# Kernel tuning notes

Measured on AMD Instinct MI355X. Metric: run time of the kernel, lower is better.

## Reference

```python
import jax, jax.numpy as jnp
import numpy as np
from jax import lax

# --- geometry constants (match init_kwargs geo) ---
NVOX = (128, 128, 128)          # (nz, ny, nx) voxels
SVOX = (256.0, 256.0, 256.0)    # volume size in mm
NDET = (256, 256)               # (V, U) detector pixels
SDET = (512.0, 512.0)           # detector size in mm
DSO = 1000.0                    # source-to-isocenter distance
DSD = 1536.0                    # source-to-detector distance
N_ANGLES = 360


def setup_inputs() -> dict:
    key = jax.random.key(0)
    # projections: [B, 1, n_angles, nDetV, nDetU]
    x = jax.random.normal(key, (2, 1, N_ANGLES, NDET[0], NDET[1]), dtype=jnp.float32)
    return {"x": x}


def _backproject(proj):
    """Voxel-driven cone-beam back-projection (adjoint of cone-beam forward projector).

    proj: [B, A, V, U] projections over a circular source trajectory.
    returns volume [B, nz, ny, nx].
    """
    B, A, V, U = proj.shape
    nz, ny, nx = NVOX
    dz, dy, dx = SVOX[0] / nz, SVOX[1] / ny, SVOX[2] / nx
    dv, du = SDET[0] / V, SDET[1] / U

    # voxel center coordinates (isocenter at origin)
    zc = ((jnp.arange(nz, dtype=jnp.float32) - (nz - 1) / 2) * dz)[:, None, None]  # [nz,1,1]
    yc = ((jnp.arange(ny, dtype=jnp.float32) - (ny - 1) / 2) * dy)[None, :, None]  # [1,ny,1]
    xc = ((jnp.arange(nx, dtype=jnp.float32) - (nx - 1) / 2) * dx)[None, None, :]  # [1,1,nx]

    angles = jnp.linspace(0.0, 2.0 * np.pi, A, endpoint=False, dtype=jnp.float32)
    proj_a = jnp.moveaxis(proj, 1, 0)  # [A, B, V, U] for scan over angles

    def bilinear(p, iv, iu):
        # p: [B, V, U]; iv, iu: [nz, ny, nx] fractional detector coords
        valid = (iu >= 0) & (iu <= U - 1) & (iv >= 0) & (iv <= V - 1)
        iu = jnp.clip(iu, 0.0, U - 1.0)
        iv = jnp.clip(iv, 0.0, V - 1.0)
        u0 = jnp.floor(iu).astype(jnp.int32)
        v0 = jnp.floor(iv).astype(jnp.int32)
        u1 = jnp.minimum(u0 + 1, U - 1)
        v1 = jnp.minimum(v0 + 1, V - 1)
        fu = iu - u0
        fv = iv - v0
        s = (p[:, v0, u0] * ((1 - fv) * (1 - fu))
             + p[:, v0, u1] * ((1 - fv) * fu)
             + p[:, v1, u0] * (fv * (1 - fu))
             + p[:, v1, u1] * (fv * fu))            # [B,nz,ny,nx]
        return s * valid.astype(p.dtype)

    def body(vol, inp):
        theta, p = inp                                # scalar, [B,V,U]
        c, s = jnp.cos(theta), jnp.sin(theta)
        xr = xc * c + yc * s                          # rotated in-plane coords [1,ny,nx]
        yr = -xc * s + yc * c                         # [1,ny,nx]
        mag = DSD / (DSO - xr)                        # perspective magnification [1,ny,nx]
        iu = jnp.broadcast_to(yr * mag / du + (U - 1) / 2, (nz, ny, nx))
        iv = zc * mag / dv + (V - 1) / 2              # [nz,ny,nx]
        vol = vol + bilinear(p, iv, iu)
        return vol, None

    vol0 = jnp.zeros((B, nz, ny, nx), dtype=proj.dtype)
    vol, _ = lax.scan(body, vol0, (angles, proj_a))
    return vol


def reference(x):
    # x: [B, 1, A, V, U] -> volume [B, 1, nz, ny, nx]
    vol = _backproject(x[:, 0])
    return vol[:, None]
```

## Files before the change

### kernel.cpp

```cpp
#include <hip/hip_runtime.h>
#include <math.h>

#define NA    360
#define ZPT   8
#define PITCH 65
#define NSTG  2048
#define VLO_MAX 224
#define ULO_MAX 191


typedef float v2f __attribute__((ext_vector_type(2)));
typedef __attribute__((address_space(1))) const void gas_t;
typedef __attribute__((address_space(3))) void las_t;

__device__ __forceinline__ int2 bbox_angle(float c, float s,
    float xclo, float xchi, float yclo, float ychi, float zvlo, float zvhi)
{
    const float a0 = xclo*c, a1 = xchi*c, b0 = yclo*s, b1 = ychi*s;
    const float xr0 = a0+b0, xr1 = a0+b1, xr2 = a1+b0, xr3 = a1+b1;
    const float xmn = fminf(fminf(xr0,xr1), fminf(xr2,xr3));
    const float xmx = fmaxf(fmaxf(xr0,xr1), fmaxf(xr2,xr3));
    const float c0 = yclo*c, c1 = ychi*c, d0 = xclo*s, d1 = xchi*s;
    const float yr0 = c0-d0, yr1 = c0-d1, yr2 = c1-d0, yr3 = c1-d1;
    const float ymn = fminf(fminf(yr0,yr1), fminf(yr2,yr3));
    const float ymx = fmaxf(fmaxf(yr0,yr1), fmaxf(yr2,yr3));
    const float mlo = 1536.f * __builtin_amdgcn_rcpf(1000.f - xmn);
    const float mhi = 1536.f * __builtin_amdgcn_rcpf(1000.f - xmx);
    const float umn = fminf(fminf(ymn*mlo, ymn*mhi), fminf(ymx*mlo, ymx*mhi));
    int u_lo = (int)floorf(fmaf(umn, 0.5f, 127.5f)) - 1;
    u_lo = u_lo < 0 ? 0 : (u_lo > ULO_MAX ? ULO_MAX : u_lo);
    const float vmn = fminf(fminf(zvlo*mlo, zvlo*mhi), fminf(zvhi*mlo, zvhi*mhi));
    int v_lo = (int)floorf(vmn + 127.5f) - 1;
    v_lo = v_lo < 0 ? 0 : (v_lo > VLO_MAX ? VLO_MAX : v_lo);
    return make_int2(u_lo, v_lo);
}

__device__ __forceinline__ void stage8(const char* gb, float* ldsw,
                                       const int goffB[8]) {
    #pragma unroll
    for (int i = 0; i < 8; ++i) {
        __builtin_amdgcn_global_load_lds(
            (gas_t*)(gb + goffB[i]),
            (las_t*)(ldsw + i * 64), 4, 0, 0);
    }
}

__device__ __forceinline__ void compute_angle(const float* __restrict__ smb,
    float c, float s, float xc, float yc, float zf0, int u_lo, int v_lo,
    v2f acc[ZPT])
{
    const float xr  = xc*c + yc*s;
    const float yr  = yc*c - xc*s;
    const float mag = 1536.f * __builtin_amdgcn_rcpf(1000.f - xr);
    const float iu  = fmaf(yr*mag, 0.5f, 127.5f);
    const bool uval = (iu >= 0.f) && (iu <= 255.f);
    const float iuc = fminf(fmaxf(iu, 0.f), 255.f);
    int u0 = (int)iuc; u0 = u0 > 254 ? 254 : u0;
    const float fu  = iuc - (float)u0;
    const float w   = uval ? 1.f : 0.f;
    const float wu1 = fu*w, wu0 = w - wu1;
    const v2f   wuv = {wu0, wu1};
    const int   ui  = u0 - u_lo;
    const float ivb = fmaf(zf0, mag, 127.5f) - (float)v_lo;
    #pragma unroll
    for (int k = 0; k < ZPT; ++k) {
        const float ivl = fmaf((float)k, mag, ivb);
        const int   v0  = (int)ivl;
        const float fv  = __builtin_amdgcn_fractf(ivl);
        const float* r  = smb + (v0 * PITCH + ui);
        v2f p0 = {r[0],     r[1]};
        v2f p1 = {r[PITCH], r[PITCH+1]};
        const v2f fvv = {fv, fv};
        const v2f q = __builtin_elementwise_fma(fvv, p1 - p0, p0);
        acc[k] = __builtin_elementwise_fma(wuv, q, acc[k]);
    }
}

__global__ __launch_bounds__(256, 4) void bp_kernel(const float* __restrict__ proj,
                                                    float* __restrict__ out) {
    __shared__ float2 cs_sh[NA];
    __shared__ int2   bb_sh[NA];
    __shared__ float  patch[2][NSTG];

    const int tid = threadIdx.y * 16 + threadIdx.x;

    const int zg = blockIdx.x;
    const int t  = blockIdx.y;
    const int b  = blockIdx.z;
    const int x0 = (t & 7) * 16;
    const int y0 = (t >> 3) * 16;
    const int zb = zg * ZPT;

    const float zf0  = (float)zb - 63.5f;
    const float xclo = ((float)x0 - 63.5f) * 2.f, xchi = xclo + 30.f;
    const float yclo = ((float)y0 - 63.5f) * 2.f, ychi = yclo + 30.f;

    for (int i = tid; i < NA; i += 256) {
        float th = (float)i * (float)(2.0 * M_PI / (double)NA);
        float sv, cv; sincosf(th, &sv, &cv);
        cs_sh[i] = make_float2(cv, sv);
        bb_sh[i] = bbox_angle(cv, sv, xclo, xchi, yclo, ychi, zf0, zf0 + 7.f);
    }
    __syncthreads();

    const int wv   = tid >> 6;
    const int lane = tid & 63;
    int goffB[8];
    #pragma unroll
    for (int i = 0; i < 8; ++i) {
        const int flat = wv * 512 + i * 64 + lane;
        const int r  = flat / PITCH;
        const int cc = flat - r * PITCH;
        goffB[i] = (r * 256 + cc) * 4;
    }

    const char* projB = (const char*)(proj + (size_t)b * (NA * 65536));
    const float xc = ((float)(x0 + threadIdx.x) - 63.5f) * 2.f;
    const float yc = ((float)(y0 + threadIdx.y) - 63.5f) * 2.f;

    float* l0 = &patch[0][wv * 512];
    float* l1 = &patch[1][wv * 512];

    v2f acc[ZPT];
    #pragma unroll
    for (int k = 0; k < ZPT; ++k) acc[k] = (v2f){0.f, 0.f};

    {
        const int2 lo = bb_sh[0];
        const uint32_t aoff = __builtin_amdgcn_readfirstlane(
            ((uint32_t)lo.y << 10) + ((uint32_t)lo.x << 2));
        stage8(projB + aoff, l0, goffB);
    }
    __syncthreads();

    for (int a = 0; a < NA; a += 2) {
        {
            const int2 lo = bb_sh[a + 1];
            const uint32_t aoff = __builtin_amdgcn_readfirstlane(
                (uint32_t)(a + 1) * 262144u +
                ((uint32_t)lo.y << 10) + ((uint32_t)lo.x << 2));
            stage8(projB + aoff, l1, goffB);
        }
        {
            const float2 cs = cs_sh[a];
            const int2   lo = bb_sh[a];
            compute_angle(patch[0], cs.x, cs.y, xc, yc, zf0, lo.x, lo.y, acc);
        }
        __syncthreads();
        if (a + 2 < NA) {
            const int2 lo = bb_sh[a + 2];
            const uint32_t aoff = __builtin_amdgcn_readfirstlane(
                (uint32_t)(a + 2) * 262144u +
                ((uint32_t)lo.y << 10) + ((uint32_t)lo.x << 2));
            stage8(projB + aoff, l0, goffB);
        }
        {
            const float2 cs = cs_sh[a + 1];
            const int2   lo = bb_sh[a + 1];
            compute_angle(patch[1], cs.x, cs.y, xc, yc, zf0, lo.x, lo.y, acc);
        }
        __syncthreads();
    }

    float* o = out + (((size_t)b * 128 + zb) * 128 + (y0 + threadIdx.y)) * 128
                   + (x0 + threadIdx.x);
    #pragma unroll
    for (int k = 0; k < ZPT; ++k) {
        o[(size_t)k * (128 * 128)] = acc[k].x + acc[k].y;
    }
}

extern "C" void kernel_launch(void* const* d_in, const int* in_sizes, int n_in,
                              void* d_out, int out_size, void* d_ws, size_t ws_size,
                              hipStream_t stream) {
    const float* proj = (const float*)d_in[0];
    float* out = (float*)d_out;
    dim3 grid(128 / ZPT, 64, 2);
    dim3 block(16, 16, 1);
    hipLaunchKernelGGL(bp_kernel, grid, block, 0, stream, proj, out);
}
```

Baseline: 843.0 us.

## Process both batches per block with interleaved LDS patch and 16-byte staging loads

Each block now handles both batch items. It stages each angle's patch from both projections into one interleaved LDS layout (rows of 128 floats, 64 columns per batch) using 16-byte global_load_lds transfers instead of 4-byte ones. The geometry, bilinear index and weight computations are shared across the two batches, and the grid is halved. The doubled LDS patch and accumulators raise register and LDS use, which may cut occupancy. The patch width drops from 65 to 64 columns, with ULO_MAX adjusted to match.

Result: faster. 785.8 us (-6.8%).

```diff
diff --git a/kernel.cpp b/kernel.cpp
--- a/kernel.cpp
+++ b/kernel.cpp
@@ -3,10 +3,10 @@
 
 #define NA    360
 #define ZPT   8
-#define PITCH 65
-#define NSTG  2048
+#define NSTG  4096
 #define VLO_MAX 224
-#define ULO_MAX 191
+#define ULO_MAX 192
+#define BSTRIDE 94371840
 
 
 typedef float v2f __attribute__((ext_vector_type(2)));
@@ -35,19 +35,19 @@
     return make_int2(u_lo, v_lo);
 }
 
-__device__ __forceinline__ void stage8(const char* gb, float* ldsw,
-                                       const int goffB[8]) {
+__device__ __forceinline__ void stage4(const char* gb, float* ldsw,
+                                       const int goffB[4]) {
     #pragma unroll
-    for (int i = 0; i < 8; ++i) {
+    for (int i = 0; i < 4; ++i) {
         __builtin_amdgcn_global_load_lds(
             (gas_t*)(gb + goffB[i]),
-            (las_t*)(ldsw + i * 64), 4, 0, 0);
+            (las_t*)(ldsw + i * 256), 16, 0, 0);
     }
 }
 
 __device__ __forceinline__ void compute_angle(const float* __restrict__ smb,
     float c, float s, float xc, float yc, float zf0, int u_lo, int v_lo,
-    v2f acc[ZPT])
+    v2f accA[ZPT], v2f accB[ZPT])
 {
     const float xr  = xc*c + yc*s;
     const float yr  = yc*c - xc*s;
@@ -67,12 +67,16 @@
         const float ivl = fmaf((float)k, mag, ivb);
         const int   v0  = (int)ivl;
         const float fv  = __builtin_amdgcn_fractf(ivl);
-        const float* r  = smb + (v0 * PITCH + ui);
-        v2f p0 = {r[0],     r[1]};
-        v2f p1 = {r[PITCH], r[PITCH+1]};
+        const float* r  = smb + ((v0 << 7) + ui);
+        const v2f a0 = {r[0],   r[1]};
+        const v2f b0 = {r[64],  r[65]};
+        const v2f a1 = {r[128], r[129]};
+        const v2f b1 = {r[192], r[193]};
         const v2f fvv = {fv, fv};
-        const v2f q = __builtin_elementwise_fma(fvv, p1 - p0, p0);
-        acc[k] = __builtin_elementwise_fma(wuv, q, acc[k]);
+        const v2f qa = __builtin_elementwise_fma(fvv, a1 - a0, a0);
+        const v2f qb = __builtin_elementwise_fma(fvv, b1 - b0, b0);
+        accA[k] = __builtin_elementwise_fma(wuv, qa, accA[k]);
+        accB[k] = __builtin_elementwise_fma(wuv, qb, accB[k]);
     }
 }
 
@@ -86,7 +90,6 @@
 
     const int zg = blockIdx.x;
     const int t  = blockIdx.y;
-    const int b  = blockIdx.z;
     const int x0 = (t & 7) * 16;
     const int y0 = (t >> 3) * 16;
     const int zb = zg * ZPT;
@@ -105,31 +108,35 @@
 
     const int wv   = tid >> 6;
     const int lane = tid & 63;
-    int goffB[8];
+    int goffB[4];
     #pragma unroll
-    for (int i = 0; i < 8; ++i) {
-        const int flat = wv * 512 + i * 64 + lane;
-        const int r  = flat / PITCH;
-        const int cc = flat - r * PITCH;
-        goffB[i] = (r * 256 + cc) * 4;
+    for (int i = 0; i < 4; ++i) {
+        const int f    = wv * 1024 + i * 256 + lane * 4;
+        const int v    = f >> 7;
+        const int bsel = (f >> 6) & 1;
+        const int col  = f & 63;
+        goffB[i] = bsel * BSTRIDE + v * 1024 + col * 4;
     }
 
-    const char* projB = (const char*)(proj + (size_t)b * (NA * 65536));
+    const char* projB = (const char*)proj;
     const float xc = ((float)(x0 + threadIdx.x) - 63.5f) * 2.f;
     const float yc = ((float)(y0 + threadIdx.y) - 63.5f) * 2.f;
 
-    float* l0 = &patch[0][wv * 512];
-    float* l1 = &patch[1][wv * 512];
+    float* l0 = &patch[0][wv * 1024];
+    float* l1 = &patch[1][wv * 1024];
 
-    v2f acc[ZPT];
+    v2f accA[ZPT], accB[ZPT];
     #pragma unroll
-    for (int k = 0; k < ZPT; ++k) acc[k] = (v2f){0.f, 0.f};
+    for (int k = 0; k < ZPT; ++k) {
+        accA[k] = (v2f){0.f, 0.f};
+        accB[k] = (v2f){0.f, 0.f};
+    }
 
     {
         const int2 lo = bb_sh[0];
         const uint32_t aoff = __builtin_amdgcn_readfirstlane(
             ((uint32_t)lo.y << 10) + ((uint32_t)lo.x << 2));
-        stage8(projB + aoff, l0, goffB);
+        stage4(projB + aoff, l0, goffB);
     }
     __syncthreads();
 
@@ -139,12 +146,13 @@
             const uint32_t aoff = __builtin_amdgcn_readfirstlane(
                 (uint32_t)(a + 1) * 262144u +
                 ((uint32_t)lo.y << 10) + ((uint32_t)lo.x << 2));
-            stage8(projB + aoff, l1, goffB);
+            stage4(projB + aoff, l1, goffB);
         }
         {
             const float2 cs = cs_sh[a];
             const int2   lo = bb_sh[a];
-            compute_angle(patch[0], cs.x, cs.y, xc, yc, zf0, lo.x, lo.y, acc);
+            compute_angle(patch[0], cs.x, cs.y, xc, yc, zf0, lo.x, lo.y,
+                          accA, accB);
         }
         __syncthreads();
         if (a + 2 < NA) {
@@ -152,21 +160,24 @@
             const uint32_t aoff = __builtin_amdgcn_readfirstlane(
                 (uint32_t)(a + 2) * 262144u +
                 ((uint32_t)lo.y << 10) + ((uint32_t)lo.x << 2));
-            stage8(projB + aoff, l0, goffB);
+            stage4(projB + aoff, l0, goffB);
         }
         {
             const float2 cs = cs_sh[a + 1];
             const int2   lo = bb_sh[a + 1];
-            compute_angle(patch[1], cs.x, cs.y, xc, yc, zf0, lo.x, lo.y, acc);
+            compute_angle(patch[1], cs.x, cs.y, xc, yc, zf0, lo.x, lo.y,
+                          accA, accB);
         }
         __syncthreads();
     }
 
-    float* o = out + (((size_t)b * 128 + zb) * 128 + (y0 + threadIdx.y)) * 128
-                   + (x0 + threadIdx.x);
+    float* o0 = out + (((size_t)zb) * 128 + (y0 + threadIdx.y)) * 128
+                    + (x0 + threadIdx.x);
+    float* o1 = o0 + (size_t)128 * 128 * 128;
     #pragma unroll
     for (int k = 0; k < ZPT; ++k) {
-        o[(size_t)k * (128 * 128)] = acc[k].x + acc[k].y;
+        o0[(size_t)k * (128 * 128)] = accA[k].x + accA[k].y;
+        o1[(size_t)k * (128 * 128)] = accB[k].x + accB[k].y;
     }
 }
 
@@ -175,7 +186,7 @@
                               hipStream_t stream) {
     const float* proj = (const float*)d_in[0];
     float* out = (float*)d_out;
-    dim3 grid(128 / ZPT, 64, 2);
+    dim3 grid(128 / ZPT, 64, 1);
     dim3 block(16, 16, 1);
     hipLaunchKernelGGL(bp_kernel, grid, block, 0, stream, proj, out);
 }
```

## Process both batch items per block with interleaved batch-pair LDS patches

Applied to the files above, without the earlier changes.

Each block now accumulates both batch elements together. It stages an interleaved (batch0, batch1) float2 patch of 24x64 detector cells per angle, so the bilinear geometry (rotation, magnification, indices, weights) is computed once and shared across the two batches. The grid is halved and each thread does twice the accumulation work per angle with the same index math. The cost is a larger LDS patch (24x64 float2 per buffer), 12 staging loads per thread instead of 8, and a narrower u-window of 64 columns, down from 65.

New measurement: 769.8 us. 1.1x faster.

```diff
diff --git a/kernel.cpp b/kernel.cpp
--- a/kernel.cpp
+++ b/kernel.cpp
@@ -3,10 +3,12 @@
 
 #define NA    360
 #define ZPT   8
-#define PITCH 65
-#define NSTG  2048
-#define VLO_MAX 224
-#define ULO_MAX 191
+#define CROWS 24
+#define CPITCH 64
+#define NCELL (CROWS*CPITCH)
+#define VLO_MAX 232
+#define ULO_MAX 192
+#define BSTRIDE 94371840
 
 
 typedef float v2f __attribute__((ext_vector_type(2)));
@@ -35,17 +37,17 @@
     return make_int2(u_lo, v_lo);
 }
 
-__device__ __forceinline__ void stage8(const char* gb, float* ldsw,
-                                       const int goffB[8]) {
+__device__ __forceinline__ void stage12(const char* gb, float* ldsw,
+                                        const int goffB[12]) {
     #pragma unroll
-    for (int i = 0; i < 8; ++i) {
+    for (int i = 0; i < 12; ++i) {
         __builtin_amdgcn_global_load_lds(
             (gas_t*)(gb + goffB[i]),
             (las_t*)(ldsw + i * 64), 4, 0, 0);
     }
 }
 
-__device__ __forceinline__ void compute_angle(const float* __restrict__ smb,
+__device__ __forceinline__ void compute_angle(const v2f* __restrict__ smb,
     float c, float s, float xc, float yc, float zf0, int u_lo, int v_lo,
     v2f acc[ZPT])
 {
@@ -59,7 +61,8 @@
     const float fu  = iuc - (float)u0;
     const float w   = uval ? 1.f : 0.f;
     const float wu1 = fu*w, wu0 = w - wu1;
-    const v2f   wuv = {wu0, wu1};
+    const v2f   w0v = {wu0, wu0};
+    const v2f   w1v = {wu1, wu1};
     const int   ui  = u0 - u_lo;
     const float ivb = fmaf(zf0, mag, 127.5f) - (float)v_lo;
     #pragma unroll
@@ -67,12 +70,16 @@
         const float ivl = fmaf((float)k, mag, ivb);
         const int   v0  = (int)ivl;
         const float fv  = __builtin_amdgcn_fractf(ivl);
-        const float* r  = smb + (v0 * PITCH + ui);
-        v2f p0 = {r[0],     r[1]};
-        v2f p1 = {r[PITCH], r[PITCH+1]};
+        const v2f* cell = smb + ((v0 << 6) + ui);
+        const v2f c00 = cell[0];
+        const v2f c10 = cell[CPITCH];
+        const v2f c01 = cell[1];
+        const v2f c11 = cell[CPITCH+1];
         const v2f fvv = {fv, fv};
-        const v2f q = __builtin_elementwise_fma(fvv, p1 - p0, p0);
-        acc[k] = __builtin_elementwise_fma(wuv, q, acc[k]);
+        const v2f q0 = __builtin_elementwise_fma(fvv, c10 - c00, c00);
+        const v2f q1 = __builtin_elementwise_fma(fvv, c11 - c01, c01);
+        acc[k] = __builtin_elementwise_fma(w0v, q0, acc[k]);
+        acc[k] = __builtin_elementwise_fma(w1v, q1, acc[k]);
     }
 }
 
@@ -80,13 +87,12 @@
                                                     float* __restrict__ out) {
     __shared__ float2 cs_sh[NA];
     __shared__ int2   bb_sh[NA];
-    __shared__ float  patch[2][NSTG];
+    __shared__ v2f    patch[2][NCELL];
 
     const int tid = threadIdx.y * 16 + threadIdx.x;
 
     const int zg = blockIdx.x;
     const int t  = blockIdx.y;
-    const int b  = blockIdx.z;
     const int x0 = (t & 7) * 16;
     const int y0 = (t >> 3) * 16;
     const int zb = zg * ZPT;
@@ -105,21 +111,22 @@
 
     const int wv   = tid >> 6;
     const int lane = tid & 63;
-    int goffB[8];
+    int goffB[12];
     #pragma unroll
-    for (int i = 0; i < 8; ++i) {
-        const int flat = wv * 512 + i * 64 + lane;
-        const int r  = flat / PITCH;
-        const int cc = flat - r * PITCH;
-        goffB[i] = (r * 256 + cc) * 4;
+    for (int i = 0; i < 12; ++i) {
+        const int f    = wv * 768 + i * 64 + lane;
+        const int bsel = f & 1;
+        const int ucol = (f >> 1) & 63;
+        const int v    = f >> 7;
+        goffB[i] = bsel * BSTRIDE + v * 1024 + ucol * 4;
     }
 
-    const char* projB = (const char*)(proj + (size_t)b * (NA * 65536));
+    const char* projB = (const char*)proj;
     const float xc = ((float)(x0 + threadIdx.x) - 63.5f) * 2.f;
     const float yc = ((float)(y0 + threadIdx.y) - 63.5f) * 2.f;
 
-    float* l0 = &patch[0][wv * 512];
-    float* l1 = &patch[1][wv * 512];
+    float* l0 = (float*)&patch[0][0] + wv * 768;
+    float* l1 = (float*)&patch[1][0] + wv * 768;
 
     v2f acc[ZPT];
     #pragma unroll
@@ -129,7 +136,7 @@
         const int2 lo = bb_sh[0];
         const uint32_t aoff = __builtin_amdgcn_readfirstlane(
             ((uint32_t)lo.y << 10) + ((uint32_t)lo.x << 2));
-        stage8(projB + aoff, l0, goffB);
+        stage12(projB + aoff, l0, goffB);
     }
     __syncthreads();
 
@@ -139,7 +146,7 @@
             const uint32_t aoff = __builtin_amdgcn_readfirstlane(
                 (uint32_t)(a + 1) * 262144u +
                 ((uint32_t)lo.y << 10) + ((uint32_t)lo.x << 2));
-            stage8(projB + aoff, l1, goffB);
+            stage12(projB + aoff, l1, goffB);
         }
         {
             const float2 cs = cs_sh[a];
@@ -152,7 +159,7 @@
             const uint32_t aoff = __builtin_amdgcn_readfirstlane(
                 (uint32_t)(a + 2) * 262144u +
                 ((uint32_t)lo.y << 10) + ((uint32_t)lo.x << 2));
-            stage8(projB + aoff, l0, goffB);
+            stage12(projB + aoff, l0, goffB);
         }
         {
             const float2 cs = cs_sh[a + 1];
@@ -162,11 +169,13 @@
         __syncthreads();
     }
 
-    float* o = out + (((size_t)b * 128 + zb) * 128 + (y0 + threadIdx.y)) * 128
-                   + (x0 + threadIdx.x);
+    float* o0 = out + (((size_t)zb) * 128 + (y0 + threadIdx.y)) * 128
+                    + (x0 + threadIdx.x);
+    float* o1 = o0 + (size_t)128 * 128 * 128;
     #pragma unroll
     for (int k = 0; k < ZPT; ++k) {
-        o[(size_t)k * (128 * 128)] = acc[k].x + acc[k].y;
+        o0[(size_t)k * (128 * 128)] = acc[k].x;
+        o1[(size_t)k * (128 * 128)] = acc[k].y;
     }
 }
 
@@ -175,7 +184,7 @@
                               hipStream_t stream) {
     const float* proj = (const float*)d_in[0];
     float* out = (float*)d_out;
-    dim3 grid(128 / ZPT, 64, 2);
+    dim3 grid(128 / ZPT, 64, 1);
     dim3 block(16, 16, 1);
     hipLaunchKernelGGL(bp_kernel, grid, block, 0, stream, proj, out);
 }
```
